# Kernel tuning notes

Measured on AMD Instinct MI355X. Metric: run time of the kernel, lower is better.

The kernel has to match this reference:

```python
import jax, jax.numpy as jnp
import numpy as np

N_NODES = 50000


def setup_inputs() -> dict:
    key = jax.random.key(0)
    k1, k2, k3, k4 = jax.random.split(key, 4)
    in_dim, out_dim, n_edges = 128, 64, 800000
    x = jax.random.normal(k1, (N_NODES, in_dim), dtype=jnp.float32)
    edge_index = jax.random.randint(k2, (2, n_edges), 0, N_NODES, dtype=jnp.int64)
    W = jax.random.normal(k3, (in_dim, out_dim), dtype=jnp.float32) * (1.0 / np.sqrt(in_dim))
    att = jax.random.normal(k4, (2 * out_dim,), dtype=jnp.float32) * (1.0 / np.sqrt(2 * out_dim))
    return {"x": x, "edge_index": edge_index, "W": W, "att": att}


def reference(x, edge_index, W, att):
    N = x.shape[0]
    F_out = W.shape[1]
    h = x @ W                                   # [N, F]
    src, dst = edge_index[0], edge_index[1]
    hs = h[src]                                 # [E, F] gather
    hd = h[dst]                                 # [E, F] gather
    # att(cat([h_src, h_dst])) == h_src @ a1 + h_dst @ a2
    a1, a2 = att[:F_out], att[F_out:]
    logit = jax.nn.leaky_relu(hs @ a1 + hd @ a2, 0.2)   # [E]
    E = logit.shape[0]
    # The original builds a dense [N, E] matrix (row d holds logit_e at col e
    # for dst[e]==d, zeros elsewhere) and softmaxes over the E axis. The
    # equivalent sparse form: denom_d = sum_{e:dst=d} exp(logit_e) + (E - deg_d)*exp(0),
    # stabilized with m_d = max(max logit over segment, 0).
    seg_max = jax.ops.segment_max(logit, dst, num_segments=N)      # -inf on empty
    m = jnp.maximum(seg_max, 0.0)                                  # include the zero cells
    exp_l = jnp.exp(logit - m[dst])                                # [E]
    seg_sum = jax.ops.segment_sum(exp_l, dst, num_segments=N)      # [N]
    deg = jax.ops.segment_sum(jnp.ones_like(logit), dst, num_segments=N)
    denom = seg_sum + (jnp.float32(E) - deg) * jnp.exp(-m)         # zeros' contribution
    w = exp_l / denom[dst]                                          # [E]
    agg = jax.ops.segment_sum(w[:, None] * hs, dst, num_segments=N)  # [N, F]
    return jax.nn.elu(agg)
```

## Files before the change

kernel.cpp:

```cpp
#include <hip/hip_runtime.h>
#include <hip/hip_bf16.h>

#define FIN 128
#define FOUT 64
#define BINW 128
#define NBINPAD 512
#define QS 2560
#define TILE 4096
#define DPQ 32
#define RCAP 768

typedef __attribute__((ext_vector_type(8))) short short8;
typedef __attribute__((ext_vector_type(4))) float f32x4;

__device__ __forceinline__ unsigned short f2bf(float f) {
    unsigned u = __float_as_uint(f);
    unsigned r = u + 0x7FFFu + ((u >> 16) & 1u);
    return (unsigned short)(r >> 16);
}

__device__ __forceinline__ float f16lo(unsigned u) {
    return (float)__builtin_bit_cast(_Float16, (unsigned short)(u & 0xFFFFu));
}
__device__ __forceinline__ float f16hi(unsigned u) {
    return (float)__builtin_bit_cast(_Float16, (unsigned short)(u >> 16));
}

__global__ __launch_bounds__(256) void k_prep(
    const float* __restrict__ W,
    unsigned short* __restrict__ Whig, unsigned short* __restrict__ Wlog,
    int* __restrict__ qcur, int nzero)
{
    const int t = threadIdx.x;
    if (blockIdx.x >= 64) {
        const int i = (blockIdx.x - 64) * 256 + t;
        if (i < nzero) qcur[i] = 0;
        return;
    }
    const int f = blockIdx.x * 256 + t;
    const int combo = f >> 9;
    const int s = combo >> 2, c = combo & 3;
    const int r = f & 511;
    const int l = r >> 3, j = r & 7;
    const int k = s * 32 + (l >> 4) * 8 + j;
    const int n = c * 16 + (l & 15);
    const float w = W[k * 64 + n];
    const unsigned short hi = f2bf(w);
    const float hif = __uint_as_float((unsigned)hi << 16);
    Whig[f] = hi;
    Wlog[f] = f2bf(w - hif);
}

__global__ __launch_bounds__(256, 8) void k_fused(
    const float* __restrict__ x, const unsigned short* __restrict__ Whig,
    const unsigned short* __restrict__ Wlog, const float* __restrict__ att,
    unsigned* __restrict__ h2, float* __restrict__ as_, float* __restrict__ ad_,
    const int* __restrict__ src, const int* __restrict__ dst,
    unsigned* __restrict__ queue, int* __restrict__ qcur,
    int N, int E, int nbins, int paBlocks)
{
    union SMem {
        struct { unsigned rec[TILE]; int hist[NBINPAD]; int comb[NBINPAD];
                 int wtot[4]; } pa;
    };
    __shared__ SMem sm;
    const int t = threadIdx.x;

    if ((int)blockIdx.x < paBlocks) {
        const int e0 = blockIdx.x * TILE;
        const int tot = (E - e0 < TILE) ? (E - e0) : TILE;
        const int wv = t >> 6, lane = t & 63;
        sm.pa.hist[t] = 0; sm.pa.hist[t + 256] = 0;
        __syncthreads();
        #pragma unroll
        for (int i = 0; i < TILE / 256; ++i) {
            const int idx = i * 256 + t;
            const int e = e0 + idx;
            if (e < E) {
                const int d = __builtin_nontemporal_load(dst + e);
                const int s = __builtin_nontemporal_load(src + e);
                sm.pa.rec[idx] = (unsigned)s | ((unsigned)d << 16);
                atomicAdd(&sm.pa.hist[d >> 7], 1);
            }
        }
        __syncthreads();
        const int b0 = 2 * t;
        const int v0 = sm.pa.hist[b0], v1 = sm.pa.hist[b0 + 1];
        const int tv = v0 + v1;
        int sc = tv;
        #pragma unroll
        for (int off = 1; off < 64; off <<= 1) {
            const int nb = __shfl_up(sc, off);
            if (lane >= off) sc += nb;
        }
        if (lane == 63) sm.pa.wtot[wv] = sc;
        __syncthreads();
        int wbase = 0;
        #pragma unroll
        for (int w = 0; w < 4; ++w) wbase += (w < wv) ? sm.pa.wtot[w] : 0;
        const int ex0 = wbase + (sc - tv);
        const int ex1 = ex0 + v0;
        int c0 = 0, c1 = 0;
        if (b0 < nbins && v0 > 0)
            c0 = b0 * QS + atomicAdd(qcur + b0, v0) - ex0;
        if (b0 + 1 < nbins && v1 > 0)
            c1 = (b0 + 1) * QS + atomicAdd(qcur + b0 + 1, v1) - ex1;
        sm.pa.hist[b0] = ex0; sm.pa.hist[b0 + 1] = ex1;
        sm.pa.comb[b0] = c0;  sm.pa.comb[b0 + 1] = c1;
        __syncthreads();
        #pragma unroll
        for (int i = 0; i < TILE / 256; ++i) {
            const int idx = i * 256 + t;
            if (idx < tot) {
                const unsigned r = sm.pa.rec[idx];
                const int b = (int)(r >> 23);
                const int pos = atomicAdd(&sm.pa.hist[b], 1);
                const int gpos = sm.pa.comb[b] + pos;
                if (gpos < (b + 1) * QS)
                    __builtin_nontemporal_store(r, queue + gpos);
            }
        }
        return;
    }

    const int bb = blockIdx.x - paBlocks;
    const int wv = t >> 6, lane = t & 63;
    const int quad = lane >> 4, mrow = lane & 15;
    const int r0 = (bb * 4 + wv) * 16;
    const int arow = r0 + mrow;
    const bool rok = arow < N;

    f32x4 acc[4] = {};

    #pragma unroll
    for (int s = 0; s < 4; ++s) {
        float xv[8];
        if (rok) {
            const float4* p = (const float4*)(x + (size_t)arow * FIN + s * 32 + quad * 8);
            const float4 u0 = p[0], u1 = p[1];
            xv[0] = u0.x; xv[1] = u0.y; xv[2] = u0.z; xv[3] = u0.w;
            xv[4] = u1.x; xv[5] = u1.y; xv[6] = u1.z; xv[7] = u1.w;
        } else {
            #pragma unroll
            for (int j = 0; j < 8; ++j) xv[j] = 0.f;
        }
        short8 ah, al;
        #pragma unroll
        for (int j = 0; j < 8; ++j) {
            const unsigned short hi = f2bf(xv[j]);
            const float hif = __uint_as_float((unsigned)hi << 16);
            ah[j] = (short)hi;
            al[j] = (short)f2bf(xv[j] - hif);
        }
        #pragma unroll
        for (int c = 0; c < 4; ++c) {
            const short8 bh = *(const short8*)&Whig[((s * 4 + c) * 64 + lane) * 8];
            const short8 bl = *(const short8*)&Wlog[((s * 4 + c) * 64 + lane) * 8];
            acc[c] = __builtin_amdgcn_mfma_f32_16x16x32_bf16(ah, bh, acc[c], 0, 0, 0);
            acc[c] = __builtin_amdgcn_mfma_f32_16x16x32_bf16(al, bh, acc[c], 0, 0, 0);
            acc[c] = __builtin_amdgcn_mfma_f32_16x16x32_bf16(ah, bl, acc[c], 0, 0, 0);
        }
    }

    float a1v[4], a2v[4];
    #pragma unroll
    for (int c = 0; c < 4; ++c) {
        a1v[c] = att[c * 16 + mrow];
        a2v[c] = att[64 + c * 16 + mrow];
    }
    #pragma unroll
    for (int reg = 0; reg < 4; ++reg) {
        float pa = 0.f, pb = 0.f;
        #pragma unroll
        for (int c = 0; c < 4; ++c) {
            pa = fmaf(acc[c][reg], a1v[c], pa);
            pb = fmaf(acc[c][reg], a2v[c], pb);
        }
        #pragma unroll
        for (int off = 1; off < 16; off <<= 1) {
            pa += __shfl_xor(pa, off);
            pb += __shfl_xor(pb, off);
        }
        const int orow = r0 + quad * 4 + reg;
        if (mrow == 0 && orow < N) {
            as_[orow] = pa;
            ad_[orow] = pb;
        }
    }

    #pragma unroll
    for (int reg = 0; reg < 4; ++reg) {
        const int orow = r0 + quad * 4 + reg;
        if (orow < N) {
            #pragma unroll
            for (int c = 0; c < 2; ++c) {
                const unsigned lo = (unsigned)__builtin_bit_cast(unsigned short,
                                        (_Float16)acc[c][reg]);
                const unsigned hi = (unsigned)__builtin_bit_cast(unsigned short,
                                        (_Float16)acc[c + 2][reg]);
                h2[(size_t)orow * 32 + c * 16 + mrow] = lo | (hi << 16);
            }
        }
    }
}

__global__ __launch_bounds__(256) void k_aggq(
    const int* __restrict__ qcur, const unsigned* __restrict__ queue,
    const float* __restrict__ as_, const float* __restrict__ ad_,
    const unsigned* __restrict__ h2, float* __restrict__ out,
    int N, float Ef)
{
    __shared__ unsigned rec[RCAP];
    __shared__ unsigned pay[RCAP];
    __shared__ float wexp[RCAP];
    __shared__ int hist[DPQ], base[DPQ], cur[DPQ];
    __shared__ float adl[DPQ];
    __shared__ int nloc;

    const int bin = blockIdx.x >> 2, q = blockIdx.x & 3;
    const int d0 = bin * BINW + q * DPQ;
    const int t = threadIdx.x;
    const int wv = t >> 6, lane = t & 63;

    if (t < DPQ) {
        hist[t] = 0;
        const int d = d0 + t;
        adl[t] = (d < N) ? ad_[d] : 0.f;
    }
    if (t == 0) nloc = 0;
    __syncthreads();

    int cnt = qcur[bin];
    if (cnt > QS) cnt = QS;

    for (int i = t; i < cnt; i += 256) {
        const unsigned r = __builtin_nontemporal_load(queue + (size_t)bin * QS + i);
        const bool m = ((int)((r >> 21) & 3) == q);
        const unsigned long long mk = __ballot(m);
        int b0 = 0;
        if (lane == 0 && mk) b0 = atomicAdd(&nloc, __popcll(mk));
        b0 = __shfl(b0, 0);
        if (m) {
            const int p = b0 + __popcll(mk & ((1ull << lane) - 1ull));
            if (p < RCAP) {
                rec[p] = r;
                atomicAdd(&hist[(r >> 16) & (DPQ - 1)], 1);
            }
        }
    }
    __syncthreads();
    int n = nloc; if (n > RCAP) n = RCAP;

    if (t < DPQ) base[t] = hist[t];
    __syncthreads();
    #pragma unroll
    for (int off = 1; off < DPQ; off <<= 1) {
        const int a = (t < DPQ && t >= off) ? base[t - off] : 0;
        __syncthreads();
        if (t < DPQ) base[t] += a;
        __syncthreads();
    }
    if (t < DPQ) { base[t] -= hist[t]; cur[t] = base[t]; }
    __syncthreads();

    for (int i = t; i < n; i += 256) {
        const unsigned r = rec[i];
        const int s  = (int)(r & 0xFFFFu);
        const int dl = (int)(r >> 16) & (DPQ - 1);
        const float z = as_[s] + adl[dl];
        const float lg = (z >= 0.f) ? z : 0.2f * z;
        const int pos = atomicAdd(&cur[dl], 1);
        pay[pos] = (unsigned)s;
        wexp[pos] = expf(lg);
    }
    __syncthreads();

    const int grp = lane >> 4, ln = lane & 15;
    const int g16 = wv * 4 + grp;
    #pragma unroll
    for (int k = 0; k < 2; ++k) {
        const int dl = g16 + k * 16;
        const int d = d0 + dl;
        const bool ok = (d < N);
        const int dg = ok ? hist[dl] : 0;
        const int bs = ok ? base[dl] : 0;

        float ss = 0.f;
        for (int j = ln; j < dg; j += 16) ss += wexp[bs + j];
        ss += __shfl_xor(ss, 8, 16);
        ss += __shfl_xor(ss, 4, 16);
        ss += __shfl_xor(ss, 2, 16);
        ss += __shfl_xor(ss, 1, 16);
        const float inv = 1.f / (ss + (Ef - (float)dg));

        float a00 = 0.f, a01 = 0.f, a10 = 0.f, a11 = 0.f;
        for (int jb = 0; jb < dg; jb += 8) {
            float w[8]; int s[8];
            #pragma unroll
            for (int u = 0; u < 8; ++u) {
                const int j = jb + u;
                if (j < dg) {
                    s[u] = (int)pay[bs + j];
                    w[u] = wexp[bs + j] * inv;
                } else { s[u] = 0; w[u] = 0.f; }
            }
            #pragma unroll
            for (int u = 0; u < 8; ++u) {
                const uint2 hp = *(const uint2*)&h2[(size_t)s[u] * 32 + 2 * ln];
                a00 += w[u] * f16lo(hp.x);
                a01 += w[u] * f16hi(hp.x);
                a10 += w[u] * f16lo(hp.y);
                a11 += w[u] * f16hi(hp.y);
            }
        }

        if (ok) {
            const float r00 = (a00 > 0.f) ? a00 : expm1f(a00);
            const float r10 = (a10 > 0.f) ? a10 : expm1f(a10);
            const float r01 = (a01 > 0.f) ? a01 : expm1f(a01);
            const float r11 = (a11 > 0.f) ? a11 : expm1f(a11);
            float2* op0 = (float2*)(out + (size_t)d * FOUT + 2 * ln);
            float2* op1 = (float2*)(out + (size_t)d * FOUT + 32 + 2 * ln);
            *op0 = make_float2(r00, r10);
            *op1 = make_float2(r01, r11);
        }
    }
}

extern "C" void kernel_launch(void* const* d_in, const int* in_sizes, int n_in,
                              void* d_out, int out_size, void* d_ws, size_t ws_size,
                              hipStream_t stream) {
    const float* x   = (const float*)d_in[0];
    const int*   ei  = (const int*)d_in[1];
    const float* W   = (const float*)d_in[2];
    const float* att = (const float*)d_in[3];

    const int N = in_sizes[0] / FIN;
    const int E = in_sizes[1] / 2;
    const int* src = ei;
    const int* dst = ei + E;

    const int NBINS = (N + BINW - 1) / BINW;

    char* ws = (char*)d_ws;
    size_t o = 0;
    auto carve = [&](size_t bytes) {
        void* p = ws + o; o += (bytes + 1023) & ~(size_t)1023; return p;
    };
    unsigned short* Whig = (unsigned short*)carve(16384 * 2);
    unsigned short* Wlog = (unsigned short*)carve(16384 * 2);
    float*          as_  = (float*)carve((size_t)N * 4);
    float*          ad_  = (float*)carve((size_t)N * 4);
    int*            qcur = (int*)carve((size_t)NBINS * 4);
    unsigned*       h2   = (unsigned*)carve((size_t)N * 32 * 4);
    unsigned*       queue = (unsigned*)carve((size_t)NBINS * QS * 4);

    float* out = (float*)d_out;

    const int paBlocks = (E + TILE - 1) / TILE;
    const int mmBlocks = (N + 63) / 64;
    const int zBlks    = (NBINS + 255) / 256;

    k_prep<<<64 + zBlks, 256, 0, stream>>>(W, Whig, Wlog, qcur, NBINS);
    k_fused<<<paBlocks + mmBlocks, 256, 0, stream>>>(
        x, Whig, Wlog, att, h2, as_, ad_, src, dst, queue, qcur, N, E, NBINS, paBlocks);
    k_aggq<<<NBINS * 4, 256, 0, stream>>>(qcur, queue, as_, ad_, h2, out, N, (float)E);
}
```

Before: 141.9 us.

## Split fused kernel into separate binning and matmul kernels with LDS-staged coalesced queue writes

Splits the fused binning-plus-matmul kernel into two separate launches, k_phaseA and k_matmul. The binning kernel gets its own shared-memory layout and halves the edge tile size. Records are first scattered into a second LDS buffer in bin-sorted order, then written to the global queue with contiguous indices, so neighbouring threads store to adjacent addresses instead of scattering. This costs an extra kernel launch and removes the overlap the fused launch gave between binning blocks and matmul blocks. The smaller tile also means more blocks and more global atomics on the bin counters.

```diff
diff --git a/kernel.cpp b/kernel.cpp
--- a/kernel.cpp
+++ b/kernel.cpp
@@ -6,7 +6,7 @@
 #define BINW 128
 #define NBINPAD 512
 #define QS 2560
-#define TILE 4096
+#define TILE 2048
 #define DPQ 32
 #define RCAP 768
 
@@ -51,82 +51,94 @@
     Wlog[f] = f2bf(w - hif);
 }
 
-__global__ __launch_bounds__(256, 8) void k_fused(
+__global__ __launch_bounds__(256) void k_phaseA(
+    const int* __restrict__ src, const int* __restrict__ dst,
+    unsigned* __restrict__ queue, int* __restrict__ qcur,
+    int E, int nbins)
+{
+    __shared__ unsigned rec[TILE];
+    __shared__ unsigned rec2[TILE];
+    __shared__ int hist[NBINPAD];
+    __shared__ int comb[NBINPAD];
+    __shared__ int wtot[4];
+
+    const int t = threadIdx.x;
+    const int wv = t >> 6, lane = t & 63;
+    const int e0 = blockIdx.x * TILE;
+    const int tot = (E - e0 < TILE) ? (E - e0) : TILE;
+
+    hist[t] = 0; hist[t + 256] = 0;
+    __syncthreads();
+
+    #pragma unroll
+    for (int i = 0; i < TILE / 256; ++i) {
+        const int idx = i * 256 + t;
+        const int e = e0 + idx;
+        if (e < E) {
+            const int d = __builtin_nontemporal_load(dst + e);
+            const int s = __builtin_nontemporal_load(src + e);
+            rec[idx] = (unsigned)s | ((unsigned)d << 16);
+            atomicAdd(&hist[d >> 7], 1);
+        }
+    }
+    __syncthreads();
+
+    const int b0 = 2 * t;
+    const int v0 = hist[b0], v1 = hist[b0 + 1];
+    const int tv = v0 + v1;
+    int sc = tv;
+    #pragma unroll
+    for (int off = 1; off < 64; off <<= 1) {
+        const int nb = __shfl_up(sc, off);
+        if (lane >= off) sc += nb;
+    }
+    if (lane == 63) wtot[wv] = sc;
+    __syncthreads();
+    int wbase = 0;
+    #pragma unroll
+    for (int w = 0; w < 4; ++w) wbase += (w < wv) ? wtot[w] : 0;
+    const int ex0 = wbase + (sc - tv);
+    const int ex1 = ex0 + v0;
+    int c0 = 0, c1 = 0;
+    if (b0 < nbins && v0 > 0)
+        c0 = b0 * QS + atomicAdd(qcur + b0, v0) - ex0;
+    if (b0 + 1 < nbins && v1 > 0)
+        c1 = (b0 + 1) * QS + atomicAdd(qcur + b0 + 1, v1) - ex1;
+    hist[b0] = ex0; hist[b0 + 1] = ex1;
+    comb[b0] = c0;  comb[b0 + 1] = c1;
+    __syncthreads();
+
+    #pragma unroll
+    for (int i = 0; i < TILE / 256; ++i) {
+        const int idx = i * 256 + t;
+        if (idx < tot) {
+            const unsigned r = rec[idx];
+            const int b = (int)(r >> 23);
+            const int pos = atomicAdd(&hist[b], 1);
+            rec2[pos] = r;
+        }
+    }
+    __syncthreads();
+
+    for (int idx = t; idx < tot; idx += 256) {
+        const unsigned r = rec2[idx];
+        const int b = (int)(r >> 23);
+        const int gpos = comb[b] + idx;
+        if (gpos < (b + 1) * QS)
+            __builtin_nontemporal_store(r, queue + gpos);
+    }
+}
+
+__global__ __launch_bounds__(256, 8) void k_matmul(
     const float* __restrict__ x, const unsigned short* __restrict__ Whig,
     const unsigned short* __restrict__ Wlog, const float* __restrict__ att,
     unsigned* __restrict__ h2, float* __restrict__ as_, float* __restrict__ ad_,
-    const int* __restrict__ src, const int* __restrict__ dst,
-    unsigned* __restrict__ queue, int* __restrict__ qcur,
-    int N, int E, int nbins, int paBlocks)
+    int N)
 {
-    union SMem {
-        struct { unsigned rec[TILE]; int hist[NBINPAD]; int comb[NBINPAD];
-                 int wtot[4]; } pa;
-    };
-    __shared__ SMem sm;
     const int t = threadIdx.x;
-
-    if ((int)blockIdx.x < paBlocks) {
-        const int e0 = blockIdx.x * TILE;
-        const int tot = (E - e0 < TILE) ? (E - e0) : TILE;
-        const int wv = t >> 6, lane = t & 63;
-        sm.pa.hist[t] = 0; sm.pa.hist[t + 256] = 0;
-        __syncthreads();
-        #pragma unroll
-        for (int i = 0; i < TILE / 256; ++i) {
-            const int idx = i * 256 + t;
-            const int e = e0 + idx;
-            if (e < E) {
-                const int d = __builtin_nontemporal_load(dst + e);
-                const int s = __builtin_nontemporal_load(src + e);
-                sm.pa.rec[idx] = (unsigned)s | ((unsigned)d << 16);
-                atomicAdd(&sm.pa.hist[d >> 7], 1);
-            }
-        }
-        __syncthreads();
-        const int b0 = 2 * t;
-        const int v0 = sm.pa.hist[b0], v1 = sm.pa.hist[b0 + 1];
-        const int tv = v0 + v1;
-        int sc = tv;
-        #pragma unroll
-        for (int off = 1; off < 64; off <<= 1) {
-            const int nb = __shfl_up(sc, off);
-            if (lane >= off) sc += nb;
-        }
-        if (lane == 63) sm.pa.wtot[wv] = sc;
-        __syncthreads();
-        int wbase = 0;
-        #pragma unroll
-        for (int w = 0; w < 4; ++w) wbase += (w < wv) ? sm.pa.wtot[w] : 0;
-        const int ex0 = wbase + (sc - tv);
-        const int ex1 = ex0 + v0;
-        int c0 = 0, c1 = 0;
-        if (b0 < nbins && v0 > 0)
-            c0 = b0 * QS + atomicAdd(qcur + b0, v0) - ex0;
-        if (b0 + 1 < nbins && v1 > 0)
-            c1 = (b0 + 1) * QS + atomicAdd(qcur + b0 + 1, v1) - ex1;
-        sm.pa.hist[b0] = ex0; sm.pa.hist[b0 + 1] = ex1;
-        sm.pa.comb[b0] = c0;  sm.pa.comb[b0 + 1] = c1;
-        __syncthreads();
-        #pragma unroll
-        for (int i = 0; i < TILE / 256; ++i) {
-            const int idx = i * 256 + t;
-            if (idx < tot) {
-                const unsigned r = sm.pa.rec[idx];
-                const int b = (int)(r >> 23);
-                const int pos = atomicAdd(&sm.pa.hist[b], 1);
-                const int gpos = sm.pa.comb[b] + pos;
-                if (gpos < (b + 1) * QS)
-                    __builtin_nontemporal_store(r, queue + gpos);
-            }
-        }
-        return;
-    }
-
-    const int bb = blockIdx.x - paBlocks;
     const int wv = t >> 6, lane = t & 63;
     const int quad = lane >> 4, mrow = lane & 15;
-    const int r0 = (bb * 4 + wv) * 16;
+    const int r0 = (blockIdx.x * 4 + wv) * 16;
     const int arow = r0 + mrow;
     const bool rok = arow < N;
 
@@ -362,7 +374,7 @@
     const int zBlks    = (NBINS + 255) / 256;
 
     k_prep<<<64 + zBlks, 256, 0, stream>>>(W, Whig, Wlog, qcur, NBINS);
-    k_fused<<<paBlocks + mmBlocks, 256, 0, stream>>>(
-        x, Whig, Wlog, att, h2, as_, ad_, src, dst, queue, qcur, N, E, NBINS, paBlocks);
+    k_phaseA<<<paBlocks, 256, 0, stream>>>(src, dst, queue, qcur, E, NBINS);
+    k_matmul<<<mmBlocks, 256, 0, stream>>>(x, Whig, Wlog, att, h2, as_, ad_, N);
     k_aggq<<<NBINS * 4, 256, 0, stream>>>(qcur, queue, as_, ad_, h2, out, N, (float)E);
 }
```

New measurement: 135.6 us. -4.4%, faster.

## Stage bin-sorted edges in LDS for coalesced queue writes and vectorize edge loads

Applied to the files above, without the earlier changes.

The edge-partition blocks now scatter records into a second shared buffer ordered by bin, then write them to the global queue in contiguous runs so stores coalesce instead of going to scattered addresses. Full tiles load src/dst with int4 vector loads. The tile is halved to 2048 to make room for the extra shared buffer, which doubles the number of partition blocks and their global atomics on the bin cursors. The int4 path also drops the nontemporal hints on those loads.

```diff
diff --git a/kernel.cpp b/kernel.cpp
--- a/kernel.cpp
+++ b/kernel.cpp
@@ -6,7 +6,7 @@
 #define BINW 128
 #define NBINPAD 512
 #define QS 2560
-#define TILE 4096
+#define TILE 2048
 #define DPQ 32
 #define RCAP 768
 
@@ -60,8 +60,8 @@
     int N, int E, int nbins, int paBlocks)
 {
     union SMem {
-        struct { unsigned rec[TILE]; int hist[NBINPAD]; int comb[NBINPAD];
-                 int wtot[4]; } pa;
+        struct { unsigned rec[TILE]; unsigned rec2[TILE];
+                 int hist[NBINPAD]; int comb[NBINPAD]; int wtot[4]; } pa;
     };
     __shared__ SMem sm;
     const int t = threadIdx.x;
@@ -70,20 +70,42 @@
         const int e0 = blockIdx.x * TILE;
         const int tot = (E - e0 < TILE) ? (E - e0) : TILE;
         const int wv = t >> 6, lane = t & 63;
+
         sm.pa.hist[t] = 0; sm.pa.hist[t + 256] = 0;
         __syncthreads();
-        #pragma unroll
-        for (int i = 0; i < TILE / 256; ++i) {
-            const int idx = i * 256 + t;
-            const int e = e0 + idx;
-            if (e < E) {
-                const int d = __builtin_nontemporal_load(dst + e);
-                const int s = __builtin_nontemporal_load(src + e);
-                sm.pa.rec[idx] = (unsigned)s | ((unsigned)d << 16);
-                atomicAdd(&sm.pa.hist[d >> 7], 1);
-            }
-        }
-        __syncthreads();
+
+        if (tot == TILE) {
+            const int4* dp = (const int4*)(dst + e0);
+            const int4* sp = (const int4*)(src + e0);
+            #pragma unroll
+            for (int i = 0; i < TILE / 1024; ++i) {
+                const int4 dv = dp[i * 256 + t];
+                const int4 sv = sp[i * 256 + t];
+                const int idx = (i * 256 + t) * 4;
+                sm.pa.rec[idx + 0] = (unsigned)sv.x | ((unsigned)dv.x << 16);
+                sm.pa.rec[idx + 1] = (unsigned)sv.y | ((unsigned)dv.y << 16);
+                sm.pa.rec[idx + 2] = (unsigned)sv.z | ((unsigned)dv.z << 16);
+                sm.pa.rec[idx + 3] = (unsigned)sv.w | ((unsigned)dv.w << 16);
+                atomicAdd(&sm.pa.hist[dv.x >> 7], 1);
+                atomicAdd(&sm.pa.hist[dv.y >> 7], 1);
+                atomicAdd(&sm.pa.hist[dv.z >> 7], 1);
+                atomicAdd(&sm.pa.hist[dv.w >> 7], 1);
+            }
+        } else {
+            #pragma unroll
+            for (int i = 0; i < TILE / 256; ++i) {
+                const int idx = i * 256 + t;
+                const int e = e0 + idx;
+                if (e < E) {
+                    const int d = __builtin_nontemporal_load(dst + e);
+                    const int s = __builtin_nontemporal_load(src + e);
+                    sm.pa.rec[idx] = (unsigned)s | ((unsigned)d << 16);
+                    atomicAdd(&sm.pa.hist[d >> 7], 1);
+                }
+            }
+        }
+        __syncthreads();
+
         const int b0 = 2 * t;
         const int v0 = sm.pa.hist[b0], v1 = sm.pa.hist[b0 + 1];
         const int tv = v0 + v1;
@@ -108,6 +130,7 @@
         sm.pa.hist[b0] = ex0; sm.pa.hist[b0 + 1] = ex1;
         sm.pa.comb[b0] = c0;  sm.pa.comb[b0 + 1] = c1;
         __syncthreads();
+
         #pragma unroll
         for (int i = 0; i < TILE / 256; ++i) {
             const int idx = i * 256 + t;
@@ -115,10 +138,17 @@
                 const unsigned r = sm.pa.rec[idx];
                 const int b = (int)(r >> 23);
                 const int pos = atomicAdd(&sm.pa.hist[b], 1);
-                const int gpos = sm.pa.comb[b] + pos;
-                if (gpos < (b + 1) * QS)
-                    __builtin_nontemporal_store(r, queue + gpos);
-            }
+                sm.pa.rec2[pos] = r;
+            }
+        }
+        __syncthreads();
+
+        for (int idx = t; idx < tot; idx += 256) {
+            const unsigned r = sm.pa.rec2[idx];
+            const int b = (int)(r >> 23);
+            const int gpos = sm.pa.comb[b] + idx;
+            if (gpos < (b + 1) * QS)
+                __builtin_nontemporal_store(r, queue + gpos);
         }
         return;
     }
```

After: 126.5 us. -10.8%, faster.
